# Kernel optimization log

Hardware: AMD Instinct MI355X
Metric: run time of the kernel (lower is better)

The kernel has to match this reference:

```python
import jax, jax.numpy as jnp
import numpy as np

B, S, D, H, L, DFF, WIN = 2, 2048, 768, 12, 2, 3072, 512
EPS = 1e-5
DH = D // H


def setup_inputs() -> dict:
    key = jax.random.key(0)
    ks = jax.random.split(key, 8)
    rn = lambda k, shape: jax.random.normal(k, shape, jnp.float32) * 0.02
    inp = {
        "src": jax.random.normal(ks[0], (B, S, D), jnp.float32),
        "qw": rn(ks[1], (L, D, D)), "qb": jnp.zeros((L, D), jnp.float32),
        "kw": rn(ks[2], (L, D, D)), "kb": jnp.zeros((L, D), jnp.float32),
        "vw": rn(ks[3], (L, D, D)), "vb": jnp.zeros((L, D), jnp.float32),
        "ow": rn(ks[4], (L, D, D)), "ob": jnp.zeros((L, D), jnp.float32),
        "w1": rn(ks[5], (L, DFF, D)), "b1": jnp.zeros((L, DFF), jnp.float32),
        "w2": rn(ks[6], (L, D, DFF)), "b2": jnp.zeros((L, D), jnp.float32),
        "g1": jnp.ones((L, D), jnp.float32), "be1": jnp.zeros((L, D), jnp.float32),
        "g2": jnp.ones((L, D), jnp.float32), "be2": jnp.zeros((L, D), jnp.float32),
    }
    return inp


def _ln(x, g, b):
    m = jnp.mean(x, axis=-1, keepdims=True)
    v = jnp.mean(jnp.square(x - m), axis=-1, keepdims=True)
    return (x - m) * jax.lax.rsqrt(v + EPS) * g + b


def _encoder(src, qw, qb, kw, kb, vw, vb, ow, ob, w1, b1, w2, b2, g1, be1, g2, be2):
    scale = DH ** -0.5
    idx = jnp.arange(S)
    # non-causal sliding window: |i - j| <= window_size // 2
    band = jnp.abs(idx[:, None] - idx[None, :]) <= (WIN // 2)
    neg = -jnp.finfo(jnp.float32).max
    x = src
    for l in range(L):
        # projections -> (B, H, S, DH)
        q = (x @ qw[l].T + qb[l]).reshape(B, S, H, DH).transpose(0, 2, 1, 3)
        k = (x @ kw[l].T + kb[l]).reshape(B, S, H, DH).transpose(0, 2, 1, 3)
        v = (x @ vw[l].T + vb[l]).reshape(B, S, H, DH).transpose(0, 2, 1, 3)
        # full dense scores then band mask (faithful to the original module)
        sim = jnp.einsum('bhid,bhjd->bhij', q * scale, k)
        sim = jnp.where(band, sim, neg)
        attn = jax.nn.softmax(sim, axis=-1)
        o = jnp.einsum('bhij,bhjd->bhid', attn, v)
        o = o.transpose(0, 2, 1, 3).reshape(B, S, D) @ ow[l].T + ob[l]
        # post-norm transformer block (norm_first=False)
        x = _ln(x + o, g1[l], be1[l])
        ff = jax.nn.relu(x @ w1[l].T + b1[l]) @ w2[l].T + b2[l]
        x = _ln(x + ff, g2[l], be2[l])
    return x


def reference(src, qw, qb, kw, kb, vw, vb, ow, ob, w1, b1, w2, b2, g1, be1, g2, be2):
    return _encoder(src, qw, qb, kw, kb, vw, vb, ow, ob, w1, b1, w2, b2, g1, be1, g2, be2)
```

## Files before the change

kernel.cpp:

```cpp
#include <hip/hip_runtime.h>
#include <math.h>

#define BATCH 2
#define SEQ   2048
#define DM    768
#define NHD   12
#define NL    2
#define DFF   3072
#define DH    64
#define HW    256
#define MR    (BATCH*SEQ)
#define EPSF  1e-5f
#define SCALE 0.125f
#define QKVS  2304

typedef __attribute__((ext_vector_type(8))) __bf16 bf16x8;
typedef __attribute__((ext_vector_type(4))) float  f32x4;

__device__ __forceinline__ ushort f2bu(float f) {
    union { __bf16 h; ushort u; } c;
    c.h = (__bf16)f;
    return c.u;
}
__device__ __forceinline__ float bu2f(ushort u) {
    union { uint u; float f; } c;
    c.u = ((uint)u) << 16;
    return c.f;
}

__device__ __forceinline__ void gload16(const ushort* g, ushort* l) {
    __builtin_amdgcn_global_load_lds(
        (const __attribute__((address_space(1))) void*)g,
        (__attribute__((address_space(3))) void*)l, 16, 0, 0);
}

__device__ __forceinline__ void xcd_swz(int& bx, int& by, int& bz) {
    const int gx = gridDim.x, gy = gridDim.y;
    const int nwg = gx * gy * gridDim.z;
    int lin = bx + gx * (by + gy * bz);
    lin = (lin & 7) * (nwg >> 3) + (lin >> 3);
    bx = lin % gx;
    int rest = lin / gx;
    by = rest % gy;
    bz = rest / gy;
}

__global__ __launch_bounds__(256) void cvt(const float* __restrict__ in,
                                           ushort* __restrict__ out, int n)
{
    int i = (blockIdx.x * 256 + threadIdx.x) * 4;
    if (i >= n) return;
    float4 v = *(const float4*)(in + i);
    ushort4 o;
    o.x = f2bu(v.x); o.y = f2bu(v.y); o.z = f2bu(v.z); o.w = f2bu(v.w);
    *(ushort4*)(out + i) = o;
}

__global__ __launch_bounds__(256) void gemm128(
    const ushort* __restrict__ A, const ushort* __restrict__ W,
    const float* __restrict__ bias, ushort* __restrict__ C,
    int M, int N, int K, int relu)
{
    __shared__ ushort As[2][128 * 32];
    __shared__ ushort Ws[2][128 * 32];

    int bxi = blockIdx.x, byi = blockIdx.y, bzi = blockIdx.z;
    xcd_swz(bxi, byi, bzi);

    const int t  = threadIdx.x;
    const int bm = byi * 128;
    const int bn = bxi * 128;

    const int w    = t >> 6;
    const int lane = t & 63;
    const int quad = lane >> 4;
    const int lrow = lane & 15;
    const int wm   = (w >> 1) * 64;
    const int wn   = (w & 1) * 64;

    const int srow = t >> 2;
    const int scol = (t & 3) * 8;
    const ushort* ag = A + (size_t)(bm + srow) * K + scol;
    const ushort* wg = W + (size_t)(bn + srow) * K + scol;

    f32x4 acc[4][4] = {};

    gload16(ag,                  &As[0][t * 8]);
    gload16(ag + (size_t)64 * K, &As[0][2048 + t * 8]);
    gload16(wg,                  &Ws[0][t * 8]);
    gload16(wg + (size_t)64 * K, &Ws[0][2048 + t * 8]);
    __syncthreads();

    int cur = 0;
    for (int k0 = 0; k0 < K; k0 += 32) {
        const int nxt = cur ^ 1;
        if (k0 + 32 < K) {
            gload16(ag + k0 + 32,                  &As[nxt][t * 8]);
            gload16(ag + (size_t)64 * K + k0 + 32, &As[nxt][2048 + t * 8]);
            gload16(wg + k0 + 32,                  &Ws[nxt][t * 8]);
            gload16(wg + (size_t)64 * K + k0 + 32, &Ws[nxt][2048 + t * 8]);
        }

        bf16x8 af[4], bfr[4];
#pragma unroll
        for (int i = 0; i < 4; ++i)
            af[i] = *(const bf16x8*)&As[cur][(wm + i * 16 + lrow) * 32 + quad * 8];
#pragma unroll
        for (int j = 0; j < 4; ++j)
            bfr[j] = *(const bf16x8*)&Ws[cur][(wn + j * 16 + lrow) * 32 + quad * 8];

#pragma unroll
        for (int i = 0; i < 4; ++i)
#pragma unroll
            for (int j = 0; j < 4; ++j)
                acc[i][j] = __builtin_amdgcn_mfma_f32_16x16x32_bf16(
                    af[i], bfr[j], acc[i][j], 0, 0, 0);
        __syncthreads();
        cur = nxt;
    }

#pragma unroll
    for (int j = 0; j < 4; ++j) {
        const int col = bn + wn + j * 16 + lrow;
        const float bv = bias[col];
#pragma unroll
        for (int i = 0; i < 4; ++i) {
            const int rb = bm + wm + i * 16 + quad * 4;
#pragma unroll
            for (int r = 0; r < 4; ++r) {
                float vv = acc[i][j][r] + bv;
                if (relu) vv = fmaxf(vv, 0.f);
                C[(size_t)(rb + r) * N + col] = f2bu(vv);
            }
        }
    }
}

__global__ __launch_bounds__(256) void gemm64(
    const ushort* __restrict__ A, const ushort* __restrict__ W,
    const float* __restrict__ bias, ushort* __restrict__ C,
    float* __restrict__ part, int M, int N, int Kc, int ldk, int relu)
{
    __shared__ ushort As[2][64 * 32];
    __shared__ ushort Ws[2][128 * 32];

    int bxi = blockIdx.x, byi = blockIdx.y, bzi = blockIdx.z;
    xcd_swz(bxi, byi, bzi);

    const int t  = threadIdx.x;
    const int bm = byi * 64;
    const int bn = bxi * 128;
    const int z  = bzi;
    const int kbase = z * Kc;

    const int w    = t >> 6;
    const int lane = t & 63;
    const int quad = lane >> 4;
    const int lrow = lane & 15;
    const int wm   = (w >> 1) * 32;
    const int wn   = (w & 1) * 64;

    const int srow = t >> 2;
    const int scol = (t & 3) * 8;
    const ushort* ag = A + (size_t)(bm + srow) * ldk + kbase + scol;
    const ushort* wg = W + (size_t)(bn + srow) * ldk + kbase + scol;

    f32x4 acc[2][4] = {};

    gload16(ag,                    &As[0][t * 8]);
    gload16(wg,                    &Ws[0][t * 8]);
    gload16(wg + (size_t)64 * ldk, &Ws[0][2048 + t * 8]);
    __syncthreads();

    int cur = 0;
    for (int k0 = 0; k0 < Kc; k0 += 32) {
        const int nxt = cur ^ 1;
        if (k0 + 32 < Kc) {
            gload16(ag + k0 + 32,                    &As[nxt][t * 8]);
            gload16(wg + k0 + 32,                    &Ws[nxt][t * 8]);
            gload16(wg + (size_t)64 * ldk + k0 + 32, &Ws[nxt][2048 + t * 8]);
        }

        bf16x8 af[2], bfr[4];
#pragma unroll
        for (int i = 0; i < 2; ++i)
            af[i] = *(const bf16x8*)&As[cur][(wm + i * 16 + lrow) * 32 + quad * 8];
#pragma unroll
        for (int j = 0; j < 4; ++j)
            bfr[j] = *(const bf16x8*)&Ws[cur][(wn + j * 16 + lrow) * 32 + quad * 8];

#pragma unroll
        for (int i = 0; i < 2; ++i)
#pragma unroll
            for (int j = 0; j < 4; ++j)
                acc[i][j] = __builtin_amdgcn_mfma_f32_16x16x32_bf16(
                    af[i], bfr[j], acc[i][j], 0, 0, 0);
        __syncthreads();
        cur = nxt;
    }

    if (gridDim.z > 1) {
        float* po = part + (size_t)z * M * N;
#pragma unroll
        for (int j = 0; j < 4; ++j) {
            const int col = bn + wn + j * 16 + lrow;
#pragma unroll
            for (int i = 0; i < 2; ++i) {
                const int rb = bm + wm + i * 16 + quad * 4;
#pragma unroll
                for (int r = 0; r < 4; ++r)
                    po[(size_t)(rb + r) * N + col] = acc[i][j][r];
            }
        }
    } else {
#pragma unroll
        for (int j = 0; j < 4; ++j) {
            const int col = bn + wn + j * 16 + lrow;
            const float bv = bias[col];
#pragma unroll
            for (int i = 0; i < 2; ++i) {
                const int rb = bm + wm + i * 16 + quad * 4;
#pragma unroll
                for (int r = 0; r < 4; ++r) {
                    float vv = acc[i][j][r] + bv;
                    if (relu) vv = fmaxf(vv, 0.f);
                    C[(size_t)(rb + r) * N + col] = f2bu(vv);
                }
            }
        }
    }
}

#define QT  64
#define NCH 9
#define KP  72

__global__ __launch_bounds__(256) void attn(
    const ushort* __restrict__ q, const ushort* __restrict__ k,
    const ushort* __restrict__ v, ushort* __restrict__ o)
{
    __shared__ ushort kv[2][64][KP];
    __shared__ ushort vt[2][64][KP];
    __shared__ ushort sc[QT][KP];

    int bxi = blockIdx.x, byi = blockIdx.y, bzi = blockIdx.z;
    xcd_swz(bxi, byi, bzi);

    const int t    = threadIdx.x;
    const int i0   = bxi * QT;
    const int h    = byi;
    const int b    = bzi;
    const size_t ibase = (size_t)b * SEQ * QKVS + (size_t)h * DH;
    const size_t obase = (size_t)b * SEQ * DM   + (size_t)h * DH;

    const int w    = t >> 6;
    const int lane = t & 63;
    const int quad = lane >> 4;
    const int lrow = lane & 15;
    const int qrow = w * 16;

    const int jstart = i0 - HW;

    const int sjj[2] = { t >> 3, (t + 256) >> 3 };
    const int sd0 = (t & 7) * 8;

#pragma unroll
    for (int e = 0; e < 2; ++e) {
        int idx = t + 256 * e;
        int qi = idx >> 3, d0 = (idx & 7) * 8;
        uint4 raw = *(const uint4*)(q + ibase + (size_t)(i0 + qi) * QKVS + d0);
        *(uint4*)&sc[qi][d0] = raw;
    }
    uint4 kr[2], vr[2];
#pragma unroll
    for (int e = 0; e < 2; ++e) {
        int j = jstart + sjj[e];
        kr[e] = make_uint4(0, 0, 0, 0);
        vr[e] = make_uint4(0, 0, 0, 0);
        if (j >= 0 && j < SEQ) {
            kr[e] = *(const uint4*)(k + ibase + (size_t)j * QKVS + sd0);
            vr[e] = *(const uint4*)(v + ibase + (size_t)j * QKVS + sd0);
        }
    }
#pragma unroll
    for (int e = 0; e < 2; ++e) {
        *(uint4*)&kv[0][sjj[e]][sd0] = kr[e];
        const ushort* u = (const ushort*)&vr[e];
#pragma unroll
        for (int x = 0; x < 8; ++x) {
            int dh  = sd0 + x;
            int blk = ((sjj[e] >> 3) ^ (dh >> 3)) & 7;
            vt[0][dh][blk * 8 + (sjj[e] & 7)] = u[x];
        }
    }
    __syncthreads();

    const bf16x8 a0 = *(const bf16x8*)&sc[qrow + lrow][quad * 8];
    const bf16x8 a1 = *(const bf16x8*)&sc[qrow + lrow][32 + quad * 8];

    float m_s = -1e20f, l_s = 0.f;
    f32x4 oacc[4] = {};

    for (int c = 0; c < NCH; ++c) {
        const int cur = c & 1;
        const int j0  = jstart + c * 64;

        if (c + 1 < NCH) {
            const int j0n = jstart + (c + 1) * 64;
#pragma unroll
            for (int e = 0; e < 2; ++e) {
                int j = j0n + sjj[e];
                kr[e] = make_uint4(0, 0, 0, 0);
                vr[e] = make_uint4(0, 0, 0, 0);
                if (j >= 0 && j < SEQ) {
                    kr[e] = *(const uint4*)(k + ibase + (size_t)j * QKVS + sd0);
                    vr[e] = *(const uint4*)(v + ibase + (size_t)j * QKVS + sd0);
                }
            }
        }

        const bool full = (c >= 1) && (c <= 7) && (j0 >= 0) && (j0 + 64 <= SEQ);
        float p[4][4];
#pragma unroll
        for (int kt = 0; kt < 4; ++kt) {
            const int krow = kt * 16;
            bf16x8 kf0 = *(const bf16x8*)&kv[cur][krow + lrow][quad * 8];
            bf16x8 kf1 = *(const bf16x8*)&kv[cur][krow + lrow][32 + quad * 8];
            f32x4 acc = {};
            acc = __builtin_amdgcn_mfma_f32_16x16x32_bf16(kf0, a0, acc, 0, 0, 0);
            acc = __builtin_amdgcn_mfma_f32_16x16x32_bf16(kf1, a1, acc, 0, 0, 0);
            if (full) {
#pragma unroll
                for (int r = 0; r < 4; ++r) p[kt][r] = acc[r] * SCALE;
            } else {
                const int ig = i0 + qrow + lrow;
#pragma unroll
                for (int r = 0; r < 4; ++r) {
                    const int jg = j0 + krow + quad * 4 + r;
                    bool ok = (jg >= 0) && (jg < SEQ) &&
                              (jg >= ig - HW) && (jg <= ig + HW);
                    p[kt][r] = ok ? acc[r] * SCALE : -1e30f;
                }
            }
        }

        float cm = p[0][0];
#pragma unroll
        for (int kt = 0; kt < 4; ++kt)
#pragma unroll
            for (int r = 0; r < 4; ++r) cm = fmaxf(cm, p[kt][r]);
        cm = fmaxf(cm, __shfl_xor(cm, 16));
        cm = fmaxf(cm, __shfl_xor(cm, 32));

        const bool resc = !__all(cm <= m_s + 8.f);
        float f = 1.f;
        if (resc) {
            const float mn = fmaxf(m_s, cm);
            f = __expf(m_s - mn);
            m_s = mn;
        }
        float cs = 0.f;
#pragma unroll
        for (int kt = 0; kt < 4; ++kt)
#pragma unroll
            for (int r = 0; r < 4; ++r) {
                float e = __expf(p[kt][r] - m_s);
                p[kt][r] = e;
                cs += e;
            }
        cs += __shfl_xor(cs, 16);
        cs += __shfl_xor(cs, 32);
        l_s = l_s * f + cs;
        if (resc) {
            float f4[4];
#pragma unroll
            for (int r = 0; r < 4; ++r) f4[r] = __shfl(f, quad * 4 + r);
#pragma unroll
            for (int nt = 0; nt < 4; ++nt)
#pragma unroll
                for (int r = 0; r < 4; ++r) oacc[nt][r] *= f4[r];
        }

#pragma unroll
        for (int kt = 0; kt < 4; ++kt) {
            ushort4 pw;
            pw.x = f2bu(p[kt][0]);
            pw.y = f2bu(p[kt][1]);
            pw.z = f2bu(p[kt][2]);
            pw.w = f2bu(p[kt][3]);
            *(ushort4*)&sc[qrow + lrow][kt * 16 + quad * 4] = pw;
        }

        bf16x8 pa0 = *(const bf16x8*)&sc[qrow + lrow][quad * 8];
        bf16x8 pa1 = *(const bf16x8*)&sc[qrow + lrow][32 + quad * 8];
#pragma unroll
        for (int nt = 0; nt < 4; ++nt) {
            const int dh  = nt * 16 + lrow;
            const int rsw = (dh >> 3) & 7;
            bf16x8 b0 = *(const bf16x8*)&vt[cur][dh][((quad)     ^ rsw) * 8];
            bf16x8 b1 = *(const bf16x8*)&vt[cur][dh][((quad + 4) ^ rsw) * 8];
            oacc[nt] = __builtin_amdgcn_mfma_f32_16x16x32_bf16(pa0, b0, oacc[nt], 0, 0, 0);
            oacc[nt] = __builtin_amdgcn_mfma_f32_16x16x32_bf16(pa1, b1, oacc[nt], 0, 0, 0);
        }

        if (c + 1 < NCH) {
            const int nxt = cur ^ 1;
#pragma unroll
            for (int e = 0; e < 2; ++e) {
                *(uint4*)&kv[nxt][sjj[e]][sd0] = kr[e];
                const ushort* u = (const ushort*)&vr[e];
#pragma unroll
                for (int x = 0; x < 8; ++x) {
                    int dh  = sd0 + x;
                    int blk = ((sjj[e] >> 3) ^ (dh >> 3)) & 7;
                    vt[nxt][dh][blk * 8 + (sjj[e] & 7)] = u[x];
                }
            }
        }
        __syncthreads();
    }

    const float inv = 1.f / l_s;
    float inv4[4];
#pragma unroll
    for (int r = 0; r < 4; ++r) inv4[r] = __shfl(inv, quad * 4 + r);
#pragma unroll
    for (int r = 0; r < 4; ++r) {
        const int qi = i0 + qrow + quad * 4 + r;
#pragma unroll
        for (int nt = 0; nt < 4; ++nt)
            o[obase + (size_t)qi * DM + nt * 16 + lrow] = f2bu(oacc[nt][r] * inv4[r]);
    }
}

__global__ __launch_bounds__(256) void add_ln_sk(
    const ushort* __restrict__ xa, const float* __restrict__ pp,
    const float* __restrict__ bias, const float* __restrict__ g,
    const float* __restrict__ be,
    ushort* __restrict__ ob, float* __restrict__ of, int fin)
{
    const int r = blockIdx.x * 4 + (threadIdx.x >> 6);
    const int t = threadIdx.x & 63;
    const size_t off = (size_t)r * DM;
    float sv[12];
    float s1 = 0.f, s2 = 0.f;
#pragma unroll
    for (int ii = 0; ii < 12; ++ii) {
        const int c = t + 64 * ii;
        float vv = bu2f(xa[off + c]) + pp[off + c]
                 + pp[(size_t)MR * DM + off + c] + bias[c];
        sv[ii] = vv; s1 += vv; s2 += vv * vv;
    }
#pragma unroll
    for (int o2 = 32; o2; o2 >>= 1) {
        s1 += __shfl_xor(s1, o2);
        s2 += __shfl_xor(s2, o2);
    }
    const float mean = s1 * (1.f / 768.f);
    const float rstd = rsqrtf(s2 * (1.f / 768.f) - mean * mean + EPSF);
#pragma unroll
    for (int ii = 0; ii < 12; ++ii) {
        const int c = t + 64 * ii;
        float v = (sv[ii] - mean) * rstd * g[c] + be[c];
        if (fin) of[off + c] = v;
        else     ob[off + c] = f2bu(v);
    }
}

extern "C" void kernel_launch(void* const* d_in, const int* in_sizes, int n_in,
                              void* d_out, int out_size, void* d_ws, size_t ws_size,
                              hipStream_t stream) {
    (void)in_sizes; (void)n_in; (void)out_size; (void)ws_size;
    const float* src = (const float*)d_in[0];
    const float* qw  = (const float*)d_in[1];
    const float* qb  = (const float*)d_in[2];
    const float* kw  = (const float*)d_in[3];
    const float* kb  = (const float*)d_in[4];
    const float* vw  = (const float*)d_in[5];
    const float* vb  = (const float*)d_in[6];
    const float* ow  = (const float*)d_in[7];
    const float* ob  = (const float*)d_in[8];
    const float* w1  = (const float*)d_in[9];
    const float* b1  = (const float*)d_in[10];
    const float* w2  = (const float*)d_in[11];
    const float* b2  = (const float*)d_in[12];
    const float* g1  = (const float*)d_in[13];
    const float* be1 = (const float*)d_in[14];
    const float* g2  = (const float*)d_in[15];
    const float* be2 = (const float*)d_in[16];

    const size_t A    = (size_t)MR * DM;
    const size_t WD1  = (size_t)DM * DM;
    const size_t WQKV = (size_t)3 * DM * DM;
    const size_t WF1  = (size_t)DFF * DM;
    const size_t WF   = (size_t)NL * WF1;

    float*  bcat = (float*)d_ws;
    ushort* p    = (ushort*)(bcat + (size_t)NL * QKVS);
    ushort* qkvwB = p; p += (size_t)NL * WQKV;
    ushort* owB   = p; p += (size_t)NL * WD1;
    ushort* w1B   = p; p += WF;
    ushort* w2B   = p; p += WF;
    ushort* xb    = p; p += A;
    ushort* qkvB  = p; p += 3 * A;
    ushort* oB    = p; p += A;
    ushort* yB    = p; p += A;
    ushort* h1    = p; p += A;
    ushort* ffh   = p;

    float* partF = (float*)qkvB;
    float* partO = (float*)ffh;

    for (int l = 0; l < NL; ++l) {
        hipMemcpyAsync(bcat + (size_t)l * QKVS + 0,    qb + (size_t)l * DM,
                       DM * sizeof(float), hipMemcpyDeviceToDevice, stream);
        hipMemcpyAsync(bcat + (size_t)l * QKVS + DM,   kb + (size_t)l * DM,
                       DM * sizeof(float), hipMemcpyDeviceToDevice, stream);
        hipMemcpyAsync(bcat + (size_t)l * QKVS + 2*DM, vb + (size_t)l * DM,
                       DM * sizeof(float), hipMemcpyDeviceToDevice, stream);
    }

    for (int l = 0; l < NL; ++l) {
        cvt<<<(int)(WD1 / 1024), 256, 0, stream>>>(
            qw + (size_t)l * WD1, qkvwB + (size_t)l * WQKV + 0,     (int)WD1);
        cvt<<<(int)(WD1 / 1024), 256, 0, stream>>>(
            kw + (size_t)l * WD1, qkvwB + (size_t)l * WQKV + WD1,   (int)WD1);
        cvt<<<(int)(WD1 / 1024), 256, 0, stream>>>(
            vw + (size_t)l * WD1, qkvwB + (size_t)l * WQKV + 2*WD1, (int)WD1);
    }
    cvt<<<(int)(NL * WD1 / 1024), 256, 0, stream>>>(ow, owB, (int)(NL * WD1));
    cvt<<<(int)(WF / 1024), 256, 0, stream>>>(w1, w1B, (int)WF);
    cvt<<<(int)(WF / 1024), 256, 0, stream>>>(w2, w2B, (int)WF);
    cvt<<<(int)(A  / 1024), 256, 0, stream>>>(src, xb, (int)A);

    const dim3 gQKV(QKVS / 128, MR / 64);
    const dim3 gOp(DM / 128, MR / 64, 2);
    const dim3 gF1(DFF / 128, MR / 128);
    const dim3 gF2(DM / 128, MR / 64, 2);
    const dim3 gA(SEQ / QT, NHD, BATCH);

    for (int l = 0; l < NL; ++l) {
        const size_t bD = (size_t)l * DM;
        const size_t bF = (size_t)l * DFF;

        gemm64<<<gQKV, 256, 0, stream>>>(xb, qkvwB + (size_t)l * WQKV,
                                         bcat + (size_t)l * QKVS, qkvB,
                                         nullptr, MR, QKVS, DM, DM, 0);
        attn<<<gA, 256, 0, stream>>>(qkvB, qkvB + DM, qkvB + 2 * DM, oB);
        gemm64<<<gOp, 256, 0, stream>>>(oB, owB + (size_t)l * WD1, nullptr,
                                        nullptr, partO, MR, DM, DM / 2, DM, 0);
        add_ln_sk<<<MR / 4, 256, 0, stream>>>(xb, partO, ob + bD,
                                              g1 + bD, be1 + bD,
                                              h1, nullptr, 0);
        gemm128<<<gF1, 256, 0, stream>>>(h1, w1B + (size_t)l * WF1, b1 + bF, ffh,
                                         MR, DFF, DM, 1);
        gemm64<<<gF2, 256, 0, stream>>>(ffh, w2B + (size_t)l * WF1, nullptr,
                                        nullptr, partF, MR, DM, DFF / 2, DFF, 0);
        if (l == NL - 1)
            add_ln_sk<<<MR / 4, 256, 0, stream>>>(h1, partF, b2 + bD,
                                                  g2 + bD, be2 + bD,
                                                  nullptr, (float*)d_out, 1);
        else
            add_ln_sk<<<MR / 4, 256, 0, stream>>>(h1, partF, b2 + bD,
                                                  g2 + bD, be2 + bD,
                                                  xb, nullptr, 0);
    }
}
```

Before: 480.2 us.

## Triple-buffer GEMM LDS staging with vmcnt waits; use 128x128 tile for QKV

Both GEMM kernels move from double to triple buffering. Each k-tile load is issued two iterations ahead, and explicit s_waitcnt vmcnt counts plus a single barrier replace the per-iteration __syncthreads, so global loads overlap more with MFMA work. The QKV projection also switches from the 64x128 kernel to the 128x128 kernel to get more reuse per block. The cost is more LDS per block, which may lower occupancy, and fewer blocks for the QKV GEMM.

```diff
diff --git a/kernel.cpp b/kernel.cpp
--- a/kernel.cpp
+++ b/kernel.cpp
@@ -56,13 +56,21 @@
     *(ushort4*)(out + i) = o;
 }
 
+#define STAGE128(bi, kt) do {                                         \
+        const int _k0 = (kt) * 32;                                    \
+        gload16(ag + _k0,                  &As[bi][t * 8]);           \
+        gload16(ag + (size_t)64 * K + _k0, &As[bi][2048 + t * 8]);    \
+        gload16(wg + _k0,                  &Ws[bi][t * 8]);           \
+        gload16(wg + (size_t)64 * K + _k0, &Ws[bi][2048 + t * 8]);    \
+    } while (0)
+
 __global__ __launch_bounds__(256) void gemm128(
     const ushort* __restrict__ A, const ushort* __restrict__ W,
     const float* __restrict__ bias, ushort* __restrict__ C,
     int M, int N, int K, int relu)
 {
-    __shared__ ushort As[2][128 * 32];
-    __shared__ ushort Ws[2][128 * 32];
+    __shared__ ushort As[3][128 * 32];
+    __shared__ ushort Ws[3][128 * 32];
 
     int bxi = blockIdx.x, byi = blockIdx.y, bzi = blockIdx.z;
     xcd_swz(bxi, byi, bzi);
@@ -84,30 +92,26 @@
     const ushort* wg = W + (size_t)(bn + srow) * K + scol;
 
     f32x4 acc[4][4] = {};
-
-    gload16(ag,                  &As[0][t * 8]);
-    gload16(ag + (size_t)64 * K, &As[0][2048 + t * 8]);
-    gload16(wg,                  &Ws[0][t * 8]);
-    gload16(wg + (size_t)64 * K, &Ws[0][2048 + t * 8]);
-    __syncthreads();
-
-    int cur = 0;
-    for (int k0 = 0; k0 < K; k0 += 32) {
-        const int nxt = cur ^ 1;
-        if (k0 + 32 < K) {
-            gload16(ag + k0 + 32,                  &As[nxt][t * 8]);
-            gload16(ag + (size_t)64 * K + k0 + 32, &As[nxt][2048 + t * 8]);
-            gload16(wg + k0 + 32,                  &Ws[nxt][t * 8]);
-            gload16(wg + (size_t)64 * K + k0 + 32, &Ws[nxt][2048 + t * 8]);
-        }
-
+    const int NT = K / 32;
+
+    STAGE128(0, 0);
+    STAGE128(1, 1);
+
+    for (int kt = 0; kt < NT; ++kt) {
+        if (kt + 1 < NT)
+            asm volatile("s_waitcnt vmcnt(4)" ::: "memory");
+        else
+            asm volatile("s_waitcnt vmcnt(0)" ::: "memory");
+        __builtin_amdgcn_s_barrier();
+
+        const int cb = kt % 3;
         bf16x8 af[4], bfr[4];
 #pragma unroll
         for (int i = 0; i < 4; ++i)
-            af[i] = *(const bf16x8*)&As[cur][(wm + i * 16 + lrow) * 32 + quad * 8];
+            af[i] = *(const bf16x8*)&As[cb][(wm + i * 16 + lrow) * 32 + quad * 8];
 #pragma unroll
         for (int j = 0; j < 4; ++j)
-            bfr[j] = *(const bf16x8*)&Ws[cur][(wn + j * 16 + lrow) * 32 + quad * 8];
+            bfr[j] = *(const bf16x8*)&Ws[cb][(wn + j * 16 + lrow) * 32 + quad * 8];
 
 #pragma unroll
         for (int i = 0; i < 4; ++i)
@@ -115,8 +119,11 @@
             for (int j = 0; j < 4; ++j)
                 acc[i][j] = __builtin_amdgcn_mfma_f32_16x16x32_bf16(
                     af[i], bfr[j], acc[i][j], 0, 0, 0);
-        __syncthreads();
-        cur = nxt;
+
+        if (kt + 2 < NT) {
+            const int sb = (kt + 2) % 3;
+            STAGE128(sb, kt + 2);
+        }
     }
 
 #pragma unroll
@@ -135,14 +142,21 @@
         }
     }
 }
+
+#define STAGE64(bi, kt) do {                                            \
+        const int _k0 = (kt) * 32;                                      \
+        gload16(ag + _k0,                    &As[bi][t * 8]);           \
+        gload16(wg + _k0,                    &Ws[bi][t * 8]);           \
+        gload16(wg + (size_t)64 * ldk + _k0, &Ws[bi][2048 + t * 8]);    \
+    } while (0)
 
 __global__ __launch_bounds__(256) void gemm64(
     const ushort* __restrict__ A, const ushort* __restrict__ W,
     const float* __restrict__ bias, ushort* __restrict__ C,
     float* __restrict__ part, int M, int N, int Kc, int ldk, int relu)
 {
-    __shared__ ushort As[2][64 * 32];
-    __shared__ ushort Ws[2][128 * 32];
+    __shared__ ushort As[3][64 * 32];
+    __shared__ ushort Ws[3][128 * 32];
 
     int bxi = blockIdx.x, byi = blockIdx.y, bzi = blockIdx.z;
     xcd_swz(bxi, byi, bzi);
@@ -166,28 +180,26 @@
     const ushort* wg = W + (size_t)(bn + srow) * ldk + kbase + scol;
 
     f32x4 acc[2][4] = {};
-
-    gload16(ag,                    &As[0][t * 8]);
-    gload16(wg,                    &Ws[0][t * 8]);
-    gload16(wg + (size_t)64 * ldk, &Ws[0][2048 + t * 8]);
-    __syncthreads();
-
-    int cur = 0;
-    for (int k0 = 0; k0 < Kc; k0 += 32) {
-        const int nxt = cur ^ 1;
-        if (k0 + 32 < Kc) {
-            gload16(ag + k0 + 32,                    &As[nxt][t * 8]);
-            gload16(wg + k0 + 32,                    &Ws[nxt][t * 8]);
-            gload16(wg + (size_t)64 * ldk + k0 + 32, &Ws[nxt][2048 + t * 8]);
-        }
-
+    const int NT = Kc / 32;
+
+    STAGE64(0, 0);
+    STAGE64(1, 1);
+
+    for (int kt = 0; kt < NT; ++kt) {
+        if (kt + 1 < NT)
+            asm volatile("s_waitcnt vmcnt(3)" ::: "memory");
+        else
+            asm volatile("s_waitcnt vmcnt(0)" ::: "memory");
+        __builtin_amdgcn_s_barrier();
+
+        const int cb = kt % 3;
         bf16x8 af[2], bfr[4];
 #pragma unroll
         for (int i = 0; i < 2; ++i)
-            af[i] = *(const bf16x8*)&As[cur][(wm + i * 16 + lrow) * 32 + quad * 8];
+            af[i] = *(const bf16x8*)&As[cb][(wm + i * 16 + lrow) * 32 + quad * 8];
 #pragma unroll
         for (int j = 0; j < 4; ++j)
-            bfr[j] = *(const bf16x8*)&Ws[cur][(wn + j * 16 + lrow) * 32 + quad * 8];
+            bfr[j] = *(const bf16x8*)&Ws[cb][(wn + j * 16 + lrow) * 32 + quad * 8];
 
 #pragma unroll
         for (int i = 0; i < 2; ++i)
@@ -195,8 +207,11 @@
             for (int j = 0; j < 4; ++j)
                 acc[i][j] = __builtin_amdgcn_mfma_f32_16x16x32_bf16(
                     af[i], bfr[j], acc[i][j], 0, 0, 0);
-        __syncthreads();
-        cur = nxt;
+
+        if (kt + 2 < NT) {
+            const int sb = (kt + 2) % 3;
+            STAGE64(sb, kt + 2);
+        }
     }
 
     if (gridDim.z > 1) {
@@ -533,7 +548,7 @@
     cvt<<<(int)(WF / 1024), 256, 0, stream>>>(w2, w2B, (int)WF);
     cvt<<<(int)(A  / 1024), 256, 0, stream>>>(src, xb, (int)A);
 
-    const dim3 gQKV(QKVS / 128, MR / 64);
+    const dim3 gQKV(QKVS / 128, MR / 128);
     const dim3 gOp(DM / 128, MR / 64, 2);
     const dim3 gF1(DFF / 128, MR / 128);
     const dim3 gF2(DM / 128, MR / 64, 2);
@@ -543,9 +558,9 @@
         const size_t bD = (size_t)l * DM;
         const size_t bF = (size_t)l * DFF;
 
-        gemm64<<<gQKV, 256, 0, stream>>>(xb, qkvwB + (size_t)l * WQKV,
-                                         bcat + (size_t)l * QKVS, qkvB,
-                                         nullptr, MR, QKVS, DM, DM, 0);
+        gemm128<<<gQKV, 256, 0, stream>>>(xb, qkvwB + (size_t)l * WQKV,
+                                          bcat + (size_t)l * QKVS, qkvB,
+                                          MR, QKVS, DM, 0);
         attn<<<gA, 256, 0, stream>>>(qkvB, qkvB + DM, qkvB + 2 * DM, oB);
         gemm64<<<gOp, 256, 0, stream>>>(oB, owB + (size_t)l * WD1, nullptr,
                                         nullptr, partO, MR, DM, DM / 2, DM, 0);
```

New measurement: 460.7 us. 1.04x faster.
